# Kernel optimization log

Hardware: AMD Instinct MI355X
Metric: run time of the kernel (lower is better)

## Reference

```python
import jax, jax.numpy as jnp
import numpy as np

D = 128      # d_model
H = 4        # heads == edge embedding dim
C = D // H   # per-head channels
L = 4        # gnn layers
N = 200000   # batched atoms
E = 400000   # batched directed bonds
G = 8000     # molecules in batch
NTASK = 1
NEG_SLOPE = 0.2


def setup_inputs() -> dict:
    key = jax.random.key(0)
    ks = jax.random.split(key, 12)
    s = 0.05
    x = jax.random.randint(ks[0], (N, 9), 0, 16)            # atom features
    edge_index = jax.random.randint(ks[1], (2, E), 0, N)    # [src; dst]
    edge_attr = jax.random.randint(ks[2], (E,), 0, 10)      # bond types
    batch_ids = jnp.sort(jax.random.randint(ks[3], (N,), 0, G))
    atom_tables = jax.random.normal(ks[4], (9, 16, D), jnp.float32) * s
    bond_table = jax.random.normal(ks[5], (10, H), jnp.float32) * s
    Wl = jax.random.normal(ks[6], (L, D, D), jnp.float32) * s   # lin_l per layer
    bl = jnp.zeros((L, D), jnp.float32)
    Wr = jax.random.normal(ks[7], (L, D, D), jnp.float32) * s   # lin_r per layer
    br = jnp.zeros((L, D), jnp.float32)
    We = jax.random.normal(ks[8], (L, H, D), jnp.float32) * s   # lin_edge (no bias)
    att = jax.random.normal(ks[9], (L, H, C), jnp.float32) * s  # attention vector a
    cb = jnp.zeros((L, D), jnp.float32)                          # conv output bias
    Wout = jax.random.normal(ks[10], (D, NTASK), jnp.float32) * s
    bout = jnp.zeros((NTASK,), jnp.float32)
    return dict(atom_tables=atom_tables, bond_table=bond_table, Wl=Wl, bl=bl,
                Wr=Wr, br=br, We=We, att=att, cb=cb, Wout=Wout, bout=bout,
                x=x, edge_index=edge_index, edge_attr=edge_attr, batch_ids=batch_ids)


def _segment_softmax(logits, seg, num_segments):
    # logits: [Ef, H], softmax over edges sharing the same target node
    m = jax.ops.segment_max(logits, seg, num_segments=num_segments)
    e = jnp.exp(logits - m[seg])
    z = jax.ops.segment_sum(e, seg, num_segments=num_segments)
    return e / (z[seg] + 1e-16)


def _forward(atom_tables, bond_table, Wl, bl, Wr, br, We, att, cb, Wout, bout,
             x, edge_index, edge_attr, batch_ids):
    # Atom encoder: sum of per-feature embeddings -> [N, D]
    h = atom_tables[jnp.arange(9)[None, :], x].sum(axis=1)
    # Bond encoder -> [E, H]
    e_emb = bond_table[edge_attr]
    src, dst = edge_index[0], edge_index[1]
    n = h.shape[0]
    # add_self_loops with fill_value='mean': per-target mean of incoming edge feats
    sums = jax.ops.segment_sum(e_emb, dst, num_segments=n)
    cnt = jax.ops.segment_sum(jnp.ones((e_emb.shape[0],), e_emb.dtype), dst,
                              num_segments=n)
    loop_attr = sums / jnp.maximum(cnt, 1.0)[:, None]
    ar = jnp.arange(n)
    src_f = jnp.concatenate([src, ar])
    dst_f = jnp.concatenate([dst, ar])
    e_full = jnp.concatenate([e_emb, loop_attr], axis=0)   # [E+N, H]

    for l in range(L):
        xl = (h @ Wl[l] + bl[l]).reshape(n, H, C)
        xr = (h @ Wr[l] + br[l]).reshape(n, H, C)
        ee = (e_full @ We[l]).reshape(-1, H, C)            # [E+N, H, C]
        g = jax.nn.leaky_relu(xl[src_f] + xr[dst_f] + ee, NEG_SLOPE)
        logits = jnp.einsum('ehc,hc->eh', g, att[l])
        alpha = _segment_softmax(logits, dst_f, n)         # [E+N, H]
        out = jax.ops.segment_sum(xl[src_f] * alpha[:, :, None], dst_f,
                                  num_segments=n)
        h = out.reshape(n, D) + cb[l]
        if l < L - 1:
            h = jax.nn.relu(h)

    # global add pool over molecules, then linear head
    pooled = jax.ops.segment_sum(h, batch_ids, num_segments=G)  # [G, D]
    return pooled @ Wout + bout                                  # [G, num_tasks]


def reference(atom_tables, bond_table, Wl, bl, Wr, br, We, att, cb, Wout, bout,
              x, edge_index, edge_attr, batch_ids):
    return _forward(atom_tables, bond_table, Wl, bl, Wr, br, We, att, cb, Wout,
                    bout, x, edge_index, edge_attr, batch_ids)
```

## Files before the change

### kernel.cpp

```cpp
#include <hip/hip_runtime.h>
#include <hip/hip_bf16.h>

#define DD 128
#define NEG 0.2f

typedef short bf16x8 __attribute__((ext_vector_type(8)));
typedef float f32x4 __attribute__((ext_vector_type(4)));

__device__ inline ushort f2bf(float x) {
  unsigned u = __float_as_uint(x);
  return (ushort)((u + 0x7FFF + ((u >> 16) & 1)) >> 16);
}
__device__ inline float bf2f(ushort u) { return __uint_as_float((unsigned)u << 16); }

__global__ void k_atom_enc(const int* __restrict__ x, const float* __restrict__ tab,
                           ushort* __restrict__ h_hi, ushort* __restrict__ h_lo, int N) {
  int idx = blockIdx.x * blockDim.x + threadIdx.x;
  if (idx >= N * DD) return;
  int n = idx >> 7, d = idx & 127;
  const int* xr = x + n * 9;
  float s = 0.f;
#pragma unroll
  for (int f = 0; f < 9; f++) s += tab[(f * 16 + xr[f]) * DD + d];
  ushort hi = f2bf(s);
  h_hi[idx] = hi;
  h_lo[idx] = f2bf(s - bf2f(hi));
}

__global__ void k_init(int* __restrict__ deg, float* __restrict__ cnt,
                       float* __restrict__ sums, int N) {
  int i = blockIdx.x * blockDim.x + threadIdx.x;
  if (i >= N) return;
  deg[i] = 1;
  cnt[i] = 0.f;
  sums[i * 4 + 0] = 0.f; sums[i * 4 + 1] = 0.f;
  sums[i * 4 + 2] = 0.f; sums[i * 4 + 3] = 0.f;
}

__global__ void k_edge_count(const int* __restrict__ ei, const int* __restrict__ eattr,
                             const float* __restrict__ btab, float* __restrict__ e_emb,
                             float* __restrict__ sums, float* __restrict__ cnt,
                             int* __restrict__ deg, int E) {
  int e = blockIdx.x * blockDim.x + threadIdx.x;
  if (e >= E) return;
  int d = ei[E + e];
  int a = eattr[e];
  float f0 = btab[a * 4 + 0], f1 = btab[a * 4 + 1];
  float f2 = btab[a * 4 + 2], f3 = btab[a * 4 + 3];
  e_emb[e * 4 + 0] = f0; e_emb[e * 4 + 1] = f1;
  e_emb[e * 4 + 2] = f2; e_emb[e * 4 + 3] = f3;
  atomicAdd(&sums[d * 4 + 0], f0);
  atomicAdd(&sums[d * 4 + 1], f1);
  atomicAdd(&sums[d * 4 + 2], f2);
  atomicAdd(&sums[d * 4 + 3], f3);
  atomicAdd(&cnt[d], 1.0f);
  atomicAdd(&deg[d], 1);
}

__global__ void k_loopattr(float* __restrict__ sums, const float* __restrict__ cnt, int N) {
  int i = blockIdx.x * blockDim.x + threadIdx.x;
  if (i >= N * 4) return;
  sums[i] = sums[i] / fmaxf(cnt[i >> 2], 1.0f);
}

__global__ void k_scan_block(const int* __restrict__ deg, int* __restrict__ bsums, int N) {
  __shared__ int sh[256];
  int t = threadIdx.x;
  int base = blockIdx.x * 2048 + t * 8;
  int tot = 0;
#pragma unroll
  for (int i = 0; i < 8; i++) tot += (base + i < N) ? deg[base + i] : 0;
  sh[t] = tot;
  __syncthreads();
  for (int off = 128; off > 0; off >>= 1) {
    if (t < off) sh[t] += sh[t + off];
    __syncthreads();
  }
  if (t == 0) bsums[blockIdx.x] = sh[0];
}

__global__ void k_scan_top(int* __restrict__ bsums, int* __restrict__ rowptr,
                           int nblk, int N) {
  if (threadIdx.x == 0 && blockIdx.x == 0) {
    int run = 0;
    for (int b = 0; b < nblk; b++) { int v = bsums[b]; bsums[b] = run; run += v; }
    rowptr[N] = run;
  }
}

__global__ void k_scan_down(const int* __restrict__ deg, const int* __restrict__ bsums,
                            int* __restrict__ rowptr, int* __restrict__ cursor, int N) {
  __shared__ int sh[256];
  int t = threadIdx.x;
  int base = blockIdx.x * 2048 + t * 8;
  int v[8]; int tot = 0;
#pragma unroll
  for (int i = 0; i < 8; i++) { v[i] = (base + i < N) ? deg[base + i] : 0; tot += v[i]; }
  sh[t] = tot;
  __syncthreads();
  for (int off = 1; off < 256; off <<= 1) {
    int xv = (t >= off) ? sh[t - off] : 0;
    __syncthreads();
    sh[t] += xv;
    __syncthreads();
  }
  int run = bsums[blockIdx.x] + sh[t] - tot;
#pragma unroll
  for (int i = 0; i < 8; i++) {
    if (base + i < N) { rowptr[base + i] = run; cursor[base + i] = run; run += v[i]; }
  }
}

__global__ void k_scatter(const int* __restrict__ ei, int* __restrict__ cursor,
                          int* __restrict__ eid, int E, int N) {
  int t = blockIdx.x * blockDim.x + threadIdx.x;
  if (t >= E + N) return;
  int d = (t < E) ? ei[E + t] : (t - E);
  int pos = atomicAdd(&cursor[d], 1);
  eid[pos] = t;
}

__global__ void k_slotfill(const int* __restrict__ eid, const int* __restrict__ ei,
                           const float* __restrict__ e_emb, const float* __restrict__ la,
                           int* __restrict__ slot_src, float* __restrict__ slot_emb,
                           int E, int total) {
  int p = blockIdx.x * blockDim.x + threadIdx.x;
  if (p >= total) return;
  int t = eid[p];
  bool re = t < E;
  int src = re ? ei[t] : (t - E);
  const float* fp = re ? &e_emb[(size_t)t * 4] : &la[(size_t)(t - E) * 4];
  slot_src[p] = src;
  *(float4*)&slot_emb[(size_t)p * 4] = *(const float4*)fp;
}

__global__ void k_wpack(const float* __restrict__ Wl, const float* __restrict__ Wr,
                        ushort* __restrict__ Bhi, ushort* __restrict__ Blo, int L) {
  int tid = blockIdx.x * blockDim.x + threadIdx.x;
  int total = L * 2 * 4 * 8 * 64;
  if (tid >= total) return;
  int lane = tid & 63;
  int nt = (tid >> 6) & 7;
  int kb = (tid >> 9) & 3;
  int mat = (tid >> 11) & 1;
  int layer = tid >> 12;
  const float* W = (mat ? Wr : Wl) + (size_t)layer * DD * DD;
  int kbase = kb * 32 + (lane >> 4) * 8;
  int n = nt * 16 + (lane & 15);
  size_t out = (size_t)(layer * 2 + mat) * 16384 +
               ((size_t)(kb * 8 + nt) * 64 + lane) * 8;
#pragma unroll
  for (int j = 0; j < 8; j++) {
    float xv = W[(size_t)(kbase + j) * DD + n];
    ushort h_ = f2bf(xv);
    float fh = __uint_as_float((unsigned)h_ << 16);
    ushort l_ = f2bf(xv - fh);
    Bhi[out + j] = h_;
    Blo[out + j] = l_;
  }
}

__global__ __launch_bounds__(256) void k_gemm2_mfma(
    const ushort* __restrict__ h_hi, const ushort* __restrict__ h_lo,
    const ushort* __restrict__ bhiL, const ushort* __restrict__ bloL,
    const ushort* __restrict__ bhiR, const ushort* __restrict__ bloR,
    const float* __restrict__ bl, const float* __restrict__ br,
    ushort* __restrict__ xlb, ushort* __restrict__ xrb, int N) {
  int t = threadIdx.x;
  int lane = t & 63, w = t >> 6;
  int A0 = blockIdx.x * 64;
  int arow = lane & 15;
  int kg = lane >> 4;

  f32x4 accL[4][2], accR[4][2];
#pragma unroll
  for (int mt = 0; mt < 4; mt++)
#pragma unroll
    for (int nti = 0; nti < 2; nti++) {
      accL[mt][nti] = (f32x4){0.f, 0.f, 0.f, 0.f};
      accR[mt][nti] = (f32x4){0.f, 0.f, 0.f, 0.f};
    }

#pragma unroll
  for (int kb = 0; kb < 4; kb++) {
    bf16x8 ahi[4], alo[4];
#pragma unroll
    for (int mt = 0; mt < 4; mt++) {
      size_t aoff = (size_t)(A0 + mt * 16 + arow) * DD + kb * 32 + kg * 8;
      ahi[mt] = *(const bf16x8*)&h_hi[aoff];
      alo[mt] = *(const bf16x8*)&h_lo[aoff];
    }
#pragma unroll
    for (int nti = 0; nti < 2; nti++) {
      int nt = w * 2 + nti;
      size_t fo = ((size_t)(kb * 8 + nt) * 64 + lane) * 8;
      bf16x8 bhl = *(const bf16x8*)(bhiL + fo);
      bf16x8 bll = *(const bf16x8*)(bloL + fo);
      bf16x8 bhr = *(const bf16x8*)(bhiR + fo);
      bf16x8 blr = *(const bf16x8*)(bloR + fo);
#pragma unroll
      for (int mt = 0; mt < 4; mt++) {
        accL[mt][nti] = __builtin_amdgcn_mfma_f32_16x16x32_bf16(ahi[mt], bhl, accL[mt][nti], 0, 0, 0);
        accR[mt][nti] = __builtin_amdgcn_mfma_f32_16x16x32_bf16(ahi[mt], bhr, accR[mt][nti], 0, 0, 0);
        accL[mt][nti] = __builtin_amdgcn_mfma_f32_16x16x32_bf16(ahi[mt], bll, accL[mt][nti], 0, 0, 0);
        accR[mt][nti] = __builtin_amdgcn_mfma_f32_16x16x32_bf16(ahi[mt], blr, accR[mt][nti], 0, 0, 0);
        accL[mt][nti] = __builtin_amdgcn_mfma_f32_16x16x32_bf16(alo[mt], bhl, accL[mt][nti], 0, 0, 0);
        accR[mt][nti] = __builtin_amdgcn_mfma_f32_16x16x32_bf16(alo[mt], bhr, accR[mt][nti], 0, 0, 0);
      }
    }
  }

  int col = lane & 15;
  int rgrp = (lane >> 4) * 4;
#pragma unroll
  for (int nti = 0; nti < 2; nti++) {
    int n = (w * 2 + nti) * 16 + col;
    float bLv = bl[n], bRv = br[n];
#pragma unroll
    for (int mt = 0; mt < 4; mt++) {
#pragma unroll
      for (int r = 0; r < 4; r++) {
        int atom = A0 + mt * 16 + rgrp + r;
        if (atom < N) {
          xlb[(size_t)atom * DD + n] = f2bf(accL[mt][nti][r] + bLv);
          xrb[(size_t)atom * DD + n] = f2bf(accR[mt][nti][r] + bRv);
        }
      }
    }
  }
}

__global__ __launch_bounds__(256) void k_attn(
    const ushort* __restrict__ xlb, const ushort* __restrict__ xrb,
    const int* __restrict__ slot_src, const float* __restrict__ slot_emb,
    const int* __restrict__ rowptr,
    const float* __restrict__ Wep, const float* __restrict__ attp,
    const float* __restrict__ cbp,
    const float* __restrict__ Woutp, const int* __restrict__ bid,
    float* __restrict__ outp,
    ushort* __restrict__ h_hi, ushort* __restrict__ h_lo,
    int N, int flags) {
  __shared__ float sv[4];
  __shared__ int   sb[4];
  int wid = threadIdx.x >> 6;
  int lane = threadIdx.x & 63;
  int n = blockIdx.x * 4 + wid;
  bool act = n < N;
  int nn = act ? n : (N - 1);
  int d0 = lane * 2;

  float we0[4], we1[4];
#pragma unroll
  for (int j = 0; j < 4; j++) {
    we0[j] = Wep[j * DD + d0];
    we1[j] = Wep[j * DD + d0 + 1];
  }
  int head = lane >> 4;
  float a0 = attp[head * 32 + (d0 & 31)];
  float a1 = attp[head * 32 + ((d0 + 1) & 31)];
  float xr0, xr1;
  {
    ushort2 u = *(const ushort2*)&xrb[(size_t)nn * DD + d0];
    xr0 = bf2f(u.x); xr1 = bf2f(u.y);
  }

  float z = 0.f, acc0 = 0.f, acc1 = 0.f;
  int r0 = rowptr[nn], r1 = rowptr[nn + 1];
  for (int p = r0; p < r1; p++) {
    int s = slot_src[p];
    float4 f = *(const float4*)&slot_emb[(size_t)p * 4];
    ushort2 u = *(const ushort2*)&xlb[(size_t)s * DD + d0];
    float xv0 = bf2f(u.x), xv1 = bf2f(u.y);
    float ee0 = f.x * we0[0] + f.y * we0[1] + f.z * we0[2] + f.w * we0[3];
    float ee1 = f.x * we1[0] + f.y * we1[1] + f.z * we1[2] + f.w * we1[3];
    float g0 = xv0 + xr0 + ee0; g0 = g0 > 0.f ? g0 : NEG * g0;
    float g1 = xv1 + xr1 + ee1; g1 = g1 > 0.f ? g1 : NEG * g1;
    float pv = g0 * a0 + g1 * a1;
    pv += __shfl_xor(pv, 1);
    pv += __shfl_xor(pv, 2);
    pv += __shfl_xor(pv, 4);
    pv += __shfl_xor(pv, 8);
    float wj = __expf(pv);
    z += wj;
    acc0 += wj * xv0;
    acc1 += wj * xv1;
  }
  float inv = 1.f / (z + 1e-16f);
  float o0 = acc0 * inv + cbp[d0];
  float o1 = acc1 * inv + cbp[d0 + 1];
  if (flags & 1) { o0 = fmaxf(o0, 0.f); o1 = fmaxf(o1, 0.f); }

  if (flags & 2) {
    float v = o0 * Woutp[d0] + o1 * Woutp[d0 + 1];
    v += __shfl_xor(v, 1);
    v += __shfl_xor(v, 2);
    v += __shfl_xor(v, 4);
    v += __shfl_xor(v, 8);
    v += __shfl_xor(v, 16);
    v += __shfl_xor(v, 32);
    if (lane == 0) {
      sv[wid] = act ? v : 0.f;
      sb[wid] = act ? bid[n] : -1;
    }
    __syncthreads();
    if (threadIdx.x == 0) {
      int i = 0;
      while (i < 4) {
        int b = sb[i];
        if (b < 0) { i++; continue; }
        float s2 = sv[i];
        int j = i + 1;
        while (j < 4 && sb[j] == b) { s2 += sv[j]; j++; }
        atomicAdd(&outp[b], s2);
        i = j;
      }
    }
  } else if (act) {
    ushort h0 = f2bf(o0), h1 = f2bf(o1);
    *(ushort2*)&h_hi[(size_t)n * DD + d0] = make_ushort2(h0, h1);
    *(ushort2*)&h_lo[(size_t)n * DD + d0] =
        make_ushort2(f2bf(o0 - bf2f(h0)), f2bf(o1 - bf2f(h1)));
  }
}

__global__ void k_head_init(float* __restrict__ out, const float* __restrict__ bout, int G) {
  int i = blockIdx.x * blockDim.x + threadIdx.x;
  if (i < G) out[i] = bout[0];
}

extern "C" void kernel_launch(void* const* d_in, const int* in_sizes, int n_in,
                              void* d_out, int out_size, void* d_ws, size_t ws_size,
                              hipStream_t stream) {
  const float* atom_tables = (const float*)d_in[0];
  const float* bond_table  = (const float*)d_in[1];
  const float* Wl   = (const float*)d_in[2];
  const float* bl   = (const float*)d_in[3];
  const float* Wr   = (const float*)d_in[4];
  const float* br   = (const float*)d_in[5];
  const float* We   = (const float*)d_in[6];
  const float* att  = (const float*)d_in[7];
  const float* cb   = (const float*)d_in[8];
  const float* Wout = (const float*)d_in[9];
  const float* bout = (const float*)d_in[10];
  const int* x      = (const int*)d_in[11];
  const int* ei     = (const int*)d_in[12];
  const int* eattr  = (const int*)d_in[13];
  const int* bid    = (const int*)d_in[14];

  int N = in_sizes[11] / 9;
  int E = in_sizes[13];
  int G = out_size;
  int L = in_sizes[3] / DD;

  char* p = (char*)d_ws;
  auto alloc = [&](size_t bytes) {
    char* r = p;
    p += (bytes + 255) & ~(size_t)255;
    return r;
  };
  ushort* h_hi     = (ushort*)alloc((size_t)(N + 64) * DD * 2);
  ushort* h_lo     = (ushort*)alloc((size_t)(N + 64) * DD * 2);
  ushort* xlb      = (ushort*)alloc((size_t)N * DD * 2);
  ushort* xrb      = (ushort*)alloc((size_t)N * DD * 2);
  float*  e_emb    = (float*)alloc((size_t)E * 4 * 4);
  float*  sums     = (float*)alloc((size_t)N * 4 * 4);
  int*    rowptr   = (int*)alloc((size_t)(N + 1) * 4);
  int*    eid      = (int*)alloc((size_t)(E + N) * 4);
  int*    slot_src = (int*)alloc((size_t)(E + N) * 4);
  float*  slot_emb = (float*)alloc((size_t)(E + N) * 4 * 4);
  float*  cnt      = (float*)alloc((size_t)N * 4);
  int*    deg      = (int*)alloc((size_t)N * 4);
  int*    cursor   = (int*)alloc((size_t)N * 4);
  int nblk = (N + 2047) / 2048;
  int*    bsums    = (int*)alloc((size_t)nblk * 4);
  ushort* Bhi      = (ushort*)alloc((size_t)L * 2 * 16384 * 2);
  ushort* Blo      = (ushort*)alloc((size_t)L * 2 * 16384 * 2);
  float*  out      = (float*)d_out;

  if ((size_t)(p - (char*)d_ws) > ws_size) return;

  hipLaunchKernelGGL(k_atom_enc, dim3((N * DD + 255) / 256), dim3(256), 0, stream,
                     x, atom_tables, h_hi, h_lo, N);
  hipLaunchKernelGGL(k_init, dim3((N + 255) / 256), dim3(256), 0, stream,
                     deg, cnt, sums, N);
  hipLaunchKernelGGL(k_edge_count, dim3((E + 255) / 256), dim3(256), 0, stream,
                     ei, eattr, bond_table, e_emb, sums, cnt, deg, E);
  hipLaunchKernelGGL(k_scan_block, dim3(nblk), dim3(256), 0, stream, deg, bsums, N);
  hipLaunchKernelGGL(k_scan_top, dim3(1), dim3(64), 0, stream, bsums, rowptr, nblk, N);
  hipLaunchKernelGGL(k_scan_down, dim3(nblk), dim3(256), 0, stream,
                     deg, bsums, rowptr, cursor, N);
  hipLaunchKernelGGL(k_scatter, dim3((E + N + 255) / 256), dim3(256), 0, stream,
                     ei, cursor, eid, E, N);
  hipLaunchKernelGGL(k_loopattr, dim3((N * 4 + 255) / 256), dim3(256), 0, stream,
                     sums, cnt, N);
  hipLaunchKernelGGL(k_slotfill, dim3((E + N + 255) / 256), dim3(256), 0, stream,
                     eid, ei, e_emb, sums, slot_src, slot_emb, E, E + N);
  {
    int total = L * 2 * 4 * 8 * 64;
    hipLaunchKernelGGL(k_wpack, dim3((total + 255) / 256), dim3(256), 0, stream,
                       Wl, Wr, Bhi, Blo, L);
  }
  hipLaunchKernelGGL(k_head_init, dim3((G + 255) / 256), dim3(256), 0, stream,
                     out, bout, G);

  for (int l = 0; l < L; l++) {
    const ushort* bhiL = Bhi + (size_t)(l * 2 + 0) * 16384;
    const ushort* bhiR = Bhi + (size_t)(l * 2 + 1) * 16384;
    const ushort* bloL = Blo + (size_t)(l * 2 + 0) * 16384;
    const ushort* bloR = Blo + (size_t)(l * 2 + 1) * 16384;
    hipLaunchKernelGGL(k_gemm2_mfma, dim3((N + 63) / 64), dim3(256), 0, stream,
                       h_hi, h_lo, bhiL, bloL, bhiR, bloR,
                       bl + (size_t)l * DD, br + (size_t)l * DD, xlb, xrb, N);
    int flags = (l < L - 1) ? 1 : 2;
    hipLaunchKernelGGL(k_attn, dim3((N + 3) / 4), dim3(256), 0, stream,
                       xlb, xrb, slot_src, slot_emb, rowptr,
                       We + (size_t)l * 4 * DD, att + (size_t)l * 4 * 32,
                       cb + (size_t)l * DD, Wout, bid, out, h_hi, h_lo, N, flags);
  }
}
```

Before: 1.218 ms.

## Stage GEMM A tiles in LDS via global_load_lds with XOR-swizzled h layout

The hidden-state hi/lo buffers are now stored in global memory with an XOR swizzle of 16-byte chunks by row. The MFMA GEMM copies the whole 64x128 A tile into LDS using direct global-to-LDS loads, then reads fragments from LDS with the matching swizzle so the reads avoid bank conflicts. The intent is to replace strided per-lane global A loads with coalesced bulk copies. In exchange each block uses 32KB of LDS, which may lower occupancy, and every producer and consumer of h must agree on the swizzle.

Measured after the change: 1.089 ms. -10.6%, faster.

```diff
diff --git a/kernel.cpp b/kernel.cpp
--- a/kernel.cpp
+++ b/kernel.cpp
@@ -12,6 +12,10 @@
   return (ushort)((u + 0x7FFF + ((u >> 16) & 1)) >> 16);
 }
 __device__ inline float bf2f(ushort u) { return __uint_as_float((unsigned)u << 16); }
+
+__device__ inline int swz_d(int n, int d) {
+  return (((d >> 3) ^ (n & 7)) << 3) | (d & 7);
+}
 
 __global__ void k_atom_enc(const int* __restrict__ x, const float* __restrict__ tab,
                            ushort* __restrict__ h_hi, ushort* __restrict__ h_lo, int N) {
@@ -23,8 +27,9 @@
 #pragma unroll
   for (int f = 0; f < 9; f++) s += tab[(f * 16 + xr[f]) * DD + d];
   ushort hi = f2bf(s);
-  h_hi[idx] = hi;
-  h_lo[idx] = f2bf(s - bf2f(hi));
+  size_t o = (size_t)n * DD + swz_d(n, d);
+  h_hi[o] = hi;
+  h_lo[o] = f2bf(s - bf2f(hi));
 }
 
 __global__ void k_init(int* __restrict__ deg, float* __restrict__ cnt,
@@ -166,9 +171,29 @@
     const ushort* __restrict__ bhiR, const ushort* __restrict__ bloR,
     const float* __restrict__ bl, const float* __restrict__ br,
     ushort* __restrict__ xlb, ushort* __restrict__ xrb, int N) {
+  __shared__ ushort sAhi[64 * 128];
+  __shared__ ushort sAlo[64 * 128];
   int t = threadIdx.x;
   int lane = t & 63, w = t >> 6;
   int A0 = blockIdx.x * 64;
+
+  {
+    const char* ghi = (const char*)(h_hi + (size_t)A0 * DD);
+    const char* glo = (const char*)(h_lo + (size_t)A0 * DD);
+#pragma unroll
+    for (int i = 0; i < 4; i++) {
+      int off = (w * 4 + i) * 1024 + lane * 16;
+      int lbase = (w * 4 + i) * 1024;
+      __builtin_amdgcn_global_load_lds(
+          (const __attribute__((address_space(1))) void*)(ghi + off),
+          (__attribute__((address_space(3))) void*)((char*)sAhi + lbase), 16, 0, 0);
+      __builtin_amdgcn_global_load_lds(
+          (const __attribute__((address_space(1))) void*)(glo + off),
+          (__attribute__((address_space(3))) void*)((char*)sAlo + lbase), 16, 0, 0);
+    }
+  }
+  __syncthreads();
+
   int arow = lane & 15;
   int kg = lane >> 4;
 
@@ -184,11 +209,12 @@
 #pragma unroll
   for (int kb = 0; kb < 4; kb++) {
     bf16x8 ahi[4], alo[4];
+    int c = kb * 4 + kg;
 #pragma unroll
     for (int mt = 0; mt < 4; mt++) {
-      size_t aoff = (size_t)(A0 + mt * 16 + arow) * DD + kb * 32 + kg * 8;
-      ahi[mt] = *(const bf16x8*)&h_hi[aoff];
-      alo[mt] = *(const bf16x8*)&h_lo[aoff];
+      int boff = (mt * 16 + arow) * 256 + ((c ^ (arow & 7)) << 4);
+      ahi[mt] = *(const bf16x8*)((const char*)sAhi + boff);
+      alo[mt] = *(const bf16x8*)((const char*)sAlo + boff);
     }
 #pragma unroll
     for (int nti = 0; nti < 2; nti++) {
@@ -316,9 +342,10 @@
       }
     }
   } else if (act) {
+    int dd = swz_d(n, d0);
     ushort h0 = f2bf(o0), h1 = f2bf(o1);
-    *(ushort2*)&h_hi[(size_t)n * DD + d0] = make_ushort2(h0, h1);
-    *(ushort2*)&h_lo[(size_t)n * DD + d0] =
+    *(ushort2*)&h_hi[(size_t)n * DD + dd] = make_ushort2(h0, h1);
+    *(ushort2*)&h_lo[(size_t)n * DD + dd] =
         make_ushort2(f2bf(o0 - bf2f(h0)), f2bf(o1 - bf2f(h1)));
   }
 }
```
